# Kernel tuning notes

Measured on AMD Instinct MI355X. Metric: run time of the kernel, lower is better.

The kernel has to match this reference:

```python
import jax, jax.numpy as jnp
import numpy as np

NUM_HEADS = 8
SIGMA = 1.0
LAMBDA_INIT = 0.1
GAMMA_INIT = 0.001


def _pos_encoding(H, W, d_model):
    # 2D sinusoidal encoding: first half encodes x (width), second half y (height)
    d = d_model // 2
    div = jnp.exp(jnp.arange(0, d, 2, dtype=jnp.float32) * (-np.log(10000.0) / d))
    xs = jnp.arange(W, dtype=jnp.float32)[:, None] * div  # (W, d//2)
    ys = jnp.arange(H, dtype=jnp.float32)[:, None] * div  # (H, d//2)
    pe_x = jnp.stack([jnp.sin(xs), jnp.cos(xs)], axis=-1).reshape(W, d)
    pe_y = jnp.stack([jnp.sin(ys), jnp.cos(ys)], axis=-1).reshape(H, d)
    pe = jnp.concatenate([
        jnp.broadcast_to(pe_x[None, :, :], (H, W, d)),
        jnp.broadcast_to(pe_y[:, None, :], (H, W, d)),
    ], axis=-1)
    return pe  # (H, W, d_model)


def _distance_map(H, W, sigma):
    # exp(-euclidean_dist / sigma) between all flattened pixel positions
    yy, xx = jnp.meshgrid(jnp.arange(H, dtype=jnp.float32), jnp.arange(W, dtype=jnp.float32), indexing='ij')
    coords = jnp.stack([yy.reshape(-1), xx.reshape(-1)], axis=-1)  # (HW, 2)
    d2 = jnp.sum((coords[:, None, :] - coords[None, :, :]) ** 2, axis=-1)
    return jnp.exp(-jnp.sqrt(d2) / sigma)  # (HW, HW)


def _conv1x1(x, w, b):
    # 1x1 conv == channel matmul; x: (B,C,H,W), w: (O,C), b: (O,)
    return jnp.einsum('bchw,oc->bohw', x, w) + b[None, :, None, None]


def setup_inputs() -> dict:
    key = jax.random.key(0)
    ks = jax.random.split(key, 9)
    B, C, H, W = 2, 256, 48, 48
    d_model = 256
    inp = {
        'x': jax.random.normal(ks[0], (B, C, H, W), dtype=jnp.float32),
        'Wq': jax.random.normal(ks[1], (d_model, C), dtype=jnp.float32) * 0.01,
        'bq': jnp.zeros((d_model,), dtype=jnp.float32),
        'Wk': jax.random.normal(ks[2], (d_model, C), dtype=jnp.float32) * 0.01,
        'bk': jnp.zeros((d_model,), dtype=jnp.float32),
        'Wv': jax.random.normal(ks[3], (d_model, C), dtype=jnp.float32) * 0.01,
        'bv': jnp.zeros((d_model,), dtype=jnp.float32),
        'Wo': jax.random.normal(ks[4], (C, d_model), dtype=jnp.float32) * 0.01,
        'bo': jnp.zeros((C,), dtype=jnp.float32),
        'lambda_dist': jnp.float32(LAMBDA_INIT),
        'gamma': jnp.float32(GAMMA_INIT),
    }
    return inp


def reference(x, Wq, bq, Wk, bk, Wv, bv, Wo, bo, lambda_dist, gamma):
    B, C, H, W = x.shape
    d_model = Wq.shape[0]
    d_k = d_model // NUM_HEADS
    pe = _pos_encoding(H, W, d_model).transpose(2, 0, 1)[None]  # (1, d_model, H, W)
    dm = _distance_map(H, W, SIGMA)                              # (HW, HW)

    q = _conv1x1(x, Wq, bq) + pe
    k = _conv1x1(x, Wk, bk) + pe
    v = _conv1x1(x, Wv, bv)

    def heads(t):
        return t.reshape(B, NUM_HEADS, d_k, H * W).transpose(0, 1, 3, 2)  # (B,h,HW,d_k)

    Q, K, V = heads(q), heads(k), heads(v)
    scores = jnp.einsum('bhnd,bhmd->bhnm', Q, K) / jnp.sqrt(jnp.float32(d_k))
    scores = scores + (lambda_dist * dm)[None, None]  # 'exp' distance prior bias
    attn = jax.nn.softmax(scores, axis=-1)
    out = jnp.einsum('bhnm,bhmd->bhnd', attn, V)
    out = out.transpose(0, 1, 3, 2).reshape(B, d_model, H, W)
    fused = gamma * out  # simple weighted fusion, single (self) branch
    return x + _conv1x1(fused, Wo, bo)
```

## Files before the change

kernel.cpp:

```cpp
#include <hip/hip_runtime.h>

#define HW 2304
#define SW 48
#define DMODEL 256
#define NHEADS 8
#define DK 32
#define BATCH 2

typedef unsigned short u16;
typedef __attribute__((ext_vector_type(8))) short short8;
typedef __attribute__((ext_vector_type(4))) float f32x4;

__device__ __forceinline__ float bf2f(u16 v) {
  union { unsigned int u; float f; } c; c.u = ((unsigned int)v) << 16; return c.f;
}
__device__ __forceinline__ float lo2f(unsigned int u) {
  union { unsigned int u; float f; } c; c.u = u << 16; return c.f;
}
__device__ __forceinline__ float hi2f(unsigned int u) {
  union { unsigned int u; float f; } c; c.u = u & 0xffff0000u; return c.f;
}
__device__ __forceinline__ u16 f2bf(float f) {
  union { unsigned int u; float f; } c; c.f = f;
  unsigned int u = c.u;
  unsigned int r = (u + 0x7FFFu + ((u >> 16) & 1u)) >> 16;
  return (u16)r;
}
__device__ __forceinline__ unsigned int pkbf(float a, float b) {
  union { float f; unsigned int u; } ca, cb;
  ca.f = a; cb.f = b;
  return __builtin_amdgcn_perm(ca.u, cb.u, 0x03020706u);
}
__device__ __forceinline__ int div48(int n) { return (n * 87382) >> 22; }
__device__ __forceinline__ int swz(int row, int k) {
  return ((row >> 4) << 12) + ((k >> 3) << 7) + ((row & 15) << 3) + (k & 7);
}

__global__ __launch_bounds__(256) void prep_kernel(
    const float* __restrict__ x,
    const float* __restrict__ Wq, const float* __restrict__ Wk,
    const float* __restrict__ Wv, const float* __restrict__ Wo,
    const float* __restrict__ lam_p,
    u16* __restrict__ xt, u16* __restrict__ Wb, u16* __restrict__ et) {
  int bid = blockIdx.x;
  int t = threadIdx.x;
  if (bid < 288) {
    int b = bid / 144, r = bid % 144;
    int c0 = (r / 36) * 64, n0 = (r % 36) * 64;
    __shared__ u16 sh[64][72];
#pragma unroll
    for (int p = 0; p < 4; ++p) {
      int row = (t >> 4) + p * 16;
      int col4 = (t & 15) * 4;
      float4 v = *(const float4*)(x + (size_t)(b * DMODEL + c0 + row) * HW +
                                  n0 + col4);
      sh[col4 + 0][row] = f2bf(v.x);
      sh[col4 + 1][row] = f2bf(v.y);
      sh[col4 + 2][row] = f2bf(v.z);
      sh[col4 + 3][row] = f2bf(v.w);
    }
    __syncthreads();
    u16* xtb = xt + (size_t)b * HW * DMODEL;
#pragma unroll
    for (int q = 0; q < 2; ++q) {
      int nrow = t >> 2;
      int c8 = (t & 3) * 8 + q * 32;
      *(uint4*)(xtb + swz(n0 + nrow, c0 + c8)) = *(const uint4*)&sh[nrow][c8];
    }
  } else if (bid < 544) {
    int idx = (bid - 288) * 1024 + t * 4;
    int which = idx >> 16, off = idx & 65535;
    int m = off >> 8, k = off & 255;
    const float* src = (which == 0) ? Wq : (which == 1) ? Wk
                       : (which == 2) ? Wv : Wo;
    float4 v = *(const float4*)(src + off);
    ushort4 ov;
    ov.x = f2bf(v.x); ov.y = f2bf(v.y); ov.z = f2bf(v.z); ov.w = f2bf(v.w);
    *(ushort4*)(Wb + which * 65536 + swz(m, k)) = ov;
  } else {
    int id = (bid - 544) * 256 + t;
    int flat = id * 8;
    int tile = flat >> 8;
    int within = flat & 255;
    int tm = tile / 144, tq = tile - tm * 144;
    int m = tm * 16 + (within >> 4);
    int q = tq * 16 + (within & 15);
    int ym = div48(m), xm = m - ym * SW;
    int yq = div48(q), xq = q - yq * SW;
    float lam = lam_p[0];
    float dy = (float)(yq - ym);
    float dy2 = dy * dy;
    u16 o[8];
#pragma unroll
    for (int j = 0; j < 8; ++j) {
      float dx = (float)(xq + j - xm);
      o[j] = f2bf(lam * __expf(-sqrtf(dy2 + dx * dx)));
    }
    *(uint4*)(et + flat) = *(const uint4*)o;
  }
}

__global__ __launch_bounds__(256) void qkv_kernel(
    const u16* __restrict__ Wb, const u16* __restrict__ xt,
    const float* __restrict__ bq, const float* __restrict__ bk,
    const float* __restrict__ bv,
    u16* __restrict__ qt, u16* __restrict__ ktb, u16* __restrict__ vb) {
  int t = threadIdx.x;
  int w = t >> 6, lane = t & 63, lo = lane & 15, quad = lane >> 4;
  int n0 = blockIdx.x * 64;
  int mb = blockIdx.y, b = blockIdx.z;
  int which = mb >> 2;
  int mrel0 = (mb & 3) * 64;
  const u16* A = Wb + which * 65536 + ((mrel0 + w * 16) >> 4) * 4096 + lo * 8;
  const float* bias = (which == 0) ? bq : (which == 1) ? bk : bv;
  const u16* Bx = xt + (size_t)b * HW * DMODEL + lo * 8;

  f32x4 acc[4] = {{0.f, 0.f, 0.f, 0.f}, {0.f, 0.f, 0.f, 0.f},
                  {0.f, 0.f, 0.f, 0.f}, {0.f, 0.f, 0.f, 0.f}};
#pragma unroll
  for (int k0 = 0; k0 < DMODEL; k0 += 32) {
    int kblk = ((k0 >> 3) + quad) << 7;
    short8 af = *(const short8*)(A + kblk);
#pragma unroll
    for (int nt = 0; nt < 4; ++nt) {
      short8 bf_ = *(const short8*)(Bx + ((n0 + nt * 16) >> 4) * 4096 + kblk);
      acc[nt] = __builtin_amdgcn_mfma_f32_16x16x32_bf16(af, bf_, acc[nt], 0, 0, 0);
    }
  }

  int mbase = mrel0 + w * 16 + quad * 4;
  if (which == 2) {
#pragma unroll
    for (int reg = 0; reg < 4; ++reg) {
      int mrel = mbase + reg;
      float bi = bias[mrel];
      u16* dst = vb + (size_t)(b * DMODEL + mrel) * HW + n0 + lo;
#pragma unroll
      for (int nt = 0; nt < 4; ++nt) dst[nt * 16] = f2bf(acc[nt][reg] + bi);
    }
  } else {
    float sc = (which == 0) ? 0.17677669529663687f : 1.0f;
    int h = mbase >> 5, d0 = mbase & 31;
    u16* base = ((which == 0) ? qt : ktb) + (size_t)(b * NHEADS + h) * HW * DK;
    float bi[4], dv[4];
    bool usecos[4], usey[4];
#pragma unroll
    for (int reg = 0; reg < 4; ++reg) {
      int mrel = mbase + reg;
      bi[reg] = bias[mrel];
      int oo = mrel & 127;
      dv[reg] = expf(-0.07195578415606394f * (float)(oo & ~1));
      usecos[reg] = (oo & 1);
      usey[reg] = (mrel >= 128);
    }
#pragma unroll
    for (int nt = 0; nt < 4; ++nt) {
      int n = n0 + nt * 16 + lo;
      int yy = div48(n), xx = n - yy * SW;
      ushort4 ov;
      float vals[4];
#pragma unroll
      for (int reg = 0; reg < 4; ++reg) {
        float tv = (usey[reg] ? (float)yy : (float)xx) * dv[reg];
        float pe = usecos[reg] ? cosf(tv) : sinf(tv);
        vals[reg] = (acc[nt][reg] + bi[reg] + pe) * sc;
      }
      ov.x = f2bf(vals[0]); ov.y = f2bf(vals[1]);
      ov.z = f2bf(vals[2]); ov.w = f2bf(vals[3]);
      *(ushort4*)(base + (size_t)n * DK + d0) = ov;
    }
  }
}

__global__ __launch_bounds__(256) void attn_kernel(
    const u16* __restrict__ qt, const u16* __restrict__ ktb,
    const u16* __restrict__ vb, const u16* __restrict__ et,
    u16* __restrict__ po_o, float* __restrict__ po_l) {
  int t = threadIdx.x;
  int w = t >> 6;
  int lane = t & 63;
  int lo = lane & 15, quad = lane >> 4;
  int n0 = blockIdx.x * 64;
  int h = blockIdx.y >> 2, kh = blockIdx.y & 3;
  int b = blockIdx.z;

  __shared__ u16 Ks[2][64 * 40];
  __shared__ u16 Vs[2][32 * 72];

  const u16* qtg = qt + (size_t)(b * NHEADS + h) * HW * DK;
  const u16* ktg = ktb + (size_t)(b * NHEADS + h) * HW * DK;
  const u16* vbg = vb + (size_t)(b * DMODEL + h * DK) * HW;

  short8 qf = *(const short8*)(qtg + (size_t)(n0 + w * 16 + lo) * DK + quad * 8);

  int srow = t >> 2;
  int sks = srow >> 5, srr = srow & 31;
  int sv = (srr < 16) ? (8 * (srr >> 2) + (srr & 3))
                      : (8 * ((srr - 16) >> 2) + 4 + ((srr - 16) & 3));
  int skey = sks * 32 + sv;
  int sc8 = (t & 3) * 8;
  int vdd = t >> 3, vmo = (t & 7) * 8;

  int tq = (n0 >> 4) + w;
  const u16* etw = et + (size_t)tq * 144 * 256 + lo * 16 + (quad & 1) * 8;
  int qh = quad >> 1;

  f32x4 o0 = {0.f, 0.f, 0.f, 0.f}, o1 = {0.f, 0.f, 0.f, 0.f};
  float lsum = 0.f;

  const int kt0 = kh * 9;
  {
    int m0 = kt0 * 64;
    *(uint4*)&Ks[0][srow * 40 + sc8] =
        *(const uint4*)(ktg + (size_t)(m0 + skey) * DK + sc8);
    *(uint4*)&Vs[0][vdd * 72 + vmo] =
        *(const uint4*)(vbg + (size_t)vdd * HW + m0 + vmo);
  }
  __syncthreads();

  for (int i = 0; i < 9; ++i) {
    int cur = i & 1;
    if (i + 1 < 9) {
      int m1 = (kt0 + i + 1) * 64;
      *(uint4*)&Ks[cur ^ 1][srow * 40 + sc8] =
          *(const uint4*)(ktg + (size_t)(m1 + skey) * DK + sc8);
      *(uint4*)&Vs[cur ^ 1][vdd * 72 + vmo] =
          *(const uint4*)(vbg + (size_t)vdd * HW + m1 + vmo);
    }

    int m0 = (kt0 + i) * 64;
    uint4 eb0 = *(const uint4*)(etw + (size_t)((m0 >> 4) + 0 + qh) * 256);
    uint4 eb1 = *(const uint4*)(etw + (size_t)((m0 >> 4) + 2 + qh) * 256);

#pragma unroll
    for (int ks = 0; ks < 2; ++ks) {
      uint4 ebv = ks ? eb1 : eb0;
      short8 kfA = *(const short8*)&Ks[cur][(ks * 32 + lo) * 40 + quad * 8];
      short8 kfB = *(const short8*)&Ks[cur][(ks * 32 + 16 + lo) * 40 + quad * 8];
      f32x4 z = {0.f, 0.f, 0.f, 0.f};
      f32x4 sA = __builtin_amdgcn_mfma_f32_16x16x32_bf16(kfA, qf, z, 0, 0, 0);
      f32x4 sB = __builtin_amdgcn_mfma_f32_16x16x32_bf16(kfB, qf, z, 0, 0, 0);
      float p0 = __expf(sA[0] + lo2f(ebv.x));
      float p1 = __expf(sA[1] + hi2f(ebv.x));
      float p2 = __expf(sA[2] + lo2f(ebv.y));
      float p3 = __expf(sA[3] + hi2f(ebv.y));
      float p4 = __expf(sB[0] + lo2f(ebv.z));
      float p5 = __expf(sB[1] + hi2f(ebv.z));
      float p6 = __expf(sB[2] + lo2f(ebv.w));
      float p7 = __expf(sB[3] + hi2f(ebv.w));
      lsum += ((p0 + p1) + (p2 + p3)) + ((p4 + p5) + (p6 + p7));
      unsigned int pk32[4] = {pkbf(p0, p1), pkbf(p2, p3),
                              pkbf(p4, p5), pkbf(p6, p7)};
      short8 pfrag = *(const short8*)pk32;
      short8 v0 = *(const short8*)&Vs[cur][lo * 72 + ks * 32 + quad * 8];
      o0 = __builtin_amdgcn_mfma_f32_16x16x32_bf16(v0, pfrag, o0, 0, 0, 0);
      short8 v1 = *(const short8*)&Vs[cur][(16 + lo) * 72 + ks * 32 + quad * 8];
      o1 = __builtin_amdgcn_mfma_f32_16x16x32_bf16(v1, pfrag, o1, 0, 0, 0);
    }
    __syncthreads();
  }

  lsum += __shfl_xor(lsum, 16);
  lsum += __shfl_xor(lsum, 32);

  int slot = (b * NHEADS + h) * 36 + blockIdx.x;
  u16* pw = po_o + (size_t)(kh * 576 + slot) * 2048 + w * 512;
  uint2 s0, s1;
  s0.x = pkbf(o0[0], o0[1]); s0.y = pkbf(o0[2], o0[3]);
  s1.x = pkbf(o1[0], o1[1]); s1.y = pkbf(o1[2], o1[3]);
  *(uint2*)(pw + lane * 4) = s0;
  *(uint2*)(pw + 256 + lane * 4) = s1;
  if (quad == 0)
    po_l[(size_t)(kh * 576 + slot) * 64 + w * 16 + lo] = lsum;
}

__global__ __launch_bounds__(256) void reduce_kernel(
    const u16* __restrict__ po_o, const float* __restrict__ po_l,
    u16* __restrict__ aot) {
  int t = threadIdx.x;
  int w = t >> 6, lane = t & 63, lo = lane & 15, quad = lane >> 4;
  int qt_ = blockIdx.x, h = blockIdx.y, b = blockIdx.z;
  int slot = (b * NHEADS + h) * 36 + qt_;

  float s0[4] = {0.f, 0.f, 0.f, 0.f}, s1[4] = {0.f, 0.f, 0.f, 0.f};
  float lt = 0.f;
#pragma unroll
  for (int kh = 0; kh < 4; ++kh) {
    const u16* p = po_o + (size_t)(kh * 576 + slot) * 2048 + w * 512;
    ushort4 a0 = *(const ushort4*)(p + lane * 4);
    ushort4 a1 = *(const ushort4*)(p + 256 + lane * 4);
    s0[0] += bf2f(a0.x); s0[1] += bf2f(a0.y);
    s0[2] += bf2f(a0.z); s0[3] += bf2f(a0.w);
    s1[0] += bf2f(a1.x); s1[1] += bf2f(a1.y);
    s1[2] += bf2f(a1.z); s1[3] += bf2f(a1.w);
    lt += po_l[(size_t)(kh * 576 + slot) * 64 + w * 16 + lo];
  }
  float inv = 1.0f / lt;

  int n = qt_ * 64 + w * 16 + lo;
  u16* aog = aot + (size_t)b * HW * DMODEL;
  ushort4 w0, w1;
  w0.x = f2bf(s0[0] * inv); w0.y = f2bf(s0[1] * inv);
  w0.z = f2bf(s0[2] * inv); w0.w = f2bf(s0[3] * inv);
  w1.x = f2bf(s1[0] * inv); w1.y = f2bf(s1[1] * inv);
  w1.z = f2bf(s1[2] * inv); w1.w = f2bf(s1[3] * inv);
  *(ushort4*)&aog[swz(n, h * DK + quad * 4)] = w0;
  *(ushort4*)&aog[swz(n, h * DK + 16 + quad * 4)] = w1;
}

__global__ __launch_bounds__(256) void out_kernel(
    const float* __restrict__ x, const u16* __restrict__ Wob,
    const float* __restrict__ bo, const float* __restrict__ gp,
    const u16* __restrict__ aot, float* __restrict__ out) {
  int t = threadIdx.x;
  int w = t >> 6, lane = t & 63, lo = lane & 15, quad = lane >> 4;
  int n0 = blockIdx.x * 64;
  int c0 = blockIdx.y * 64;
  int b = blockIdx.z;
  float gamma = gp[0];
  const u16* A = Wob + ((c0 + w * 16) >> 4) * 4096 + lo * 8;
  const u16* Ba = aot + (size_t)b * HW * DMODEL + lo * 8;

  f32x4 acc[4] = {{0.f, 0.f, 0.f, 0.f}, {0.f, 0.f, 0.f, 0.f},
                  {0.f, 0.f, 0.f, 0.f}, {0.f, 0.f, 0.f, 0.f}};
#pragma unroll
  for (int k0 = 0; k0 < DMODEL; k0 += 32) {
    int kblk = ((k0 >> 3) + quad) << 7;
    short8 af = *(const short8*)(A + kblk);
#pragma unroll
    for (int nt = 0; nt < 4; ++nt) {
      short8 bf_ = *(const short8*)(Ba + ((n0 + nt * 16) >> 4) * 4096 + kblk);
      acc[nt] = __builtin_amdgcn_mfma_f32_16x16x32_bf16(af, bf_, acc[nt], 0, 0, 0);
    }
  }

#pragma unroll
  for (int reg = 0; reg < 4; ++reg) {
    int c = c0 + w * 16 + quad * 4 + reg;
    float bi = bo[c];
    const float* xs = x + (size_t)(b * DMODEL + c) * HW + n0 + lo;
    float* os = out + (size_t)(b * DMODEL + c) * HW + n0 + lo;
#pragma unroll
    for (int nt = 0; nt < 4; ++nt)
      os[nt * 16] = xs[nt * 16] + gamma * acc[nt][reg] + bi;
  }
}

extern "C" void kernel_launch(void* const* d_in, const int* in_sizes, int n_in,
                              void* d_out, int out_size, void* d_ws,
                              size_t ws_size, hipStream_t stream) {
  const float* x   = (const float*)d_in[0];
  const float* Wq  = (const float*)d_in[1];
  const float* bq  = (const float*)d_in[2];
  const float* Wk  = (const float*)d_in[3];
  const float* bk  = (const float*)d_in[4];
  const float* Wv  = (const float*)d_in[5];
  const float* bv  = (const float*)d_in[6];
  const float* Wo  = (const float*)d_in[7];
  const float* bo  = (const float*)d_in[8];
  const float* lam = (const float*)d_in[9];
  const float* gam = (const float*)d_in[10];

  char* wsb = (char*)d_ws;
  u16* Wb  = (u16*)(wsb + 36864);
  u16* xt  = (u16*)(wsb + 561152);
  u16* aot = xt;
  u16* qt  = (u16*)(wsb + 2920448);
  u16* ktb = (u16*)(wsb + 5279744);
  u16* vb  = (u16*)(wsb + 7639040);
  u16* et  = (u16*)(wsb + 9998336);
  u16* po_o = (u16*)(wsb + 20615168);
  float* po_l = (float*)(wsb + 30052352);
  float* out = (float*)d_out;

  prep_kernel<<<dim3(3136), 256, 0, stream>>>(x, Wq, Wk, Wv, Wo, lam,
                                              xt, Wb, et);
  qkv_kernel<<<dim3(36, 12, BATCH), 256, 0, stream>>>(Wb, xt, bq, bk, bv,
                                                      qt, ktb, vb);
  attn_kernel<<<dim3(36, 32, BATCH), 256, 0, stream>>>(qt, ktb, vb, et,
                                                       po_o, po_l);
  reduce_kernel<<<dim3(36, 8, BATCH), 256, 0, stream>>>(po_o, po_l, aot);
  out_kernel<<<dim3(36, 4, BATCH), 256, 0, stream>>>(x, Wb + 3 * 65536, bo, gam,
                                                     aot, out);
}
```

Baseline: 129.6 us.

## Compress distance bias table, use exp2 with bias-initialized MFMA, fuse reduce into output GEMM

Replaces the full HW×HW distance-bias table with a compact table indexed by relative (dy, dx) tile offsets, so prep_kernel launches far fewer blocks and the attention kernel reads a small cached table. The attention loop folds log2e into Q and lambda, seeds the score MFMA accumulator with the bias, uses exp2, and computes the row sum with a ones-matrix MFMA instead of scalar adds and shuffles. The separate reduce kernel is removed; out_kernel now merges the four key-split partials per head into shared memory before its projection GEMM, which saves a launch and a round trip through the aot buffer. Fast sin, cos and exp intrinsics are used in the QKV epilogue, which slightly lowers accuracy.

```diff
diff --git a/kernel.cpp b/kernel.cpp
--- a/kernel.cpp
+++ b/kernel.cpp
@@ -31,10 +31,20 @@
   ca.f = a; cb.f = b;
   return __builtin_amdgcn_perm(ca.u, cb.u, 0x03020706u);
 }
+__device__ __forceinline__ float ex2(float x) {
+#if __has_builtin(__builtin_amdgcn_exp2f)
+  return __builtin_amdgcn_exp2f(x);
+#else
+  return __expf(x * 0.6931471805599453f);
+#endif
+}
 __device__ __forceinline__ int div48(int n) { return (n * 87382) >> 22; }
+__device__ __forceinline__ int div3(int n) { return (n * 171) >> 9; }
 __device__ __forceinline__ int swz(int row, int k) {
   return ((row >> 4) << 12) + ((k >> 3) << 7) + ((row & 15) << 3) + (k & 7);
 }
+
+#define LOG2E 1.4426950408889634f
 
 __global__ __launch_bounds__(256) void prep_kernel(
     const float* __restrict__ x,
@@ -79,24 +89,26 @@
     *(ushort4*)(Wb + which * 65536 + swz(m, k)) = ov;
   } else {
     int id = (bid - 544) * 256 + t;
-    int flat = id * 8;
-    int tile = flat >> 8;
-    int within = flat & 255;
-    int tm = tile / 144, tq = tile - tm * 144;
-    int m = tm * 16 + (within >> 4);
-    int q = tq * 16 + (within & 15);
-    int ym = div48(m), xm = m - ym * SW;
-    int yq = div48(q), xq = q - yq * SW;
-    float lam = lam_p[0];
-    float dy = (float)(yq - ym);
-    float dy2 = dy * dy;
-    u16 o[8];
-#pragma unroll
-    for (int j = 0; j < 8; ++j) {
-      float dx = (float)(xq + j - xm);
-      o[j] = f2bf(lam * __expf(-sqrtf(dy2 + dx * dx)));
-    }
-    *(uint4*)(et + flat) = *(const uint4*)o;
+    if (id < 15200) {
+      int flat = id * 8;
+      int tile = flat >> 8;
+      int within = flat & 255;
+      int a = within >> 4;
+      int b0 = within & 15;
+      int dyi = (tile * 205) >> 10;
+      int dp = tile - dyi * 5;
+      float dy = (float)(dyi - 47);
+      float dy2 = dy * dy;
+      int dxb = (dp - 2) * 16 + a - b0;
+      float lam = lam_p[0] * LOG2E;
+      u16 o[8];
+#pragma unroll
+      for (int j = 0; j < 8; ++j) {
+        float dx = (float)(dxb - j);
+        o[j] = f2bf(lam * __expf(-sqrtf(dy2 + dx * dx)));
+      }
+      *(uint4*)(et + flat) = *(const uint4*)o;
+    }
   }
 }
 
@@ -139,7 +151,7 @@
       for (int nt = 0; nt < 4; ++nt) dst[nt * 16] = f2bf(acc[nt][reg] + bi);
     }
   } else {
-    float sc = (which == 0) ? 0.17677669529663687f : 1.0f;
+    float sc = (which == 0) ? (0.17677669529663687f * LOG2E) : 1.0f;
     int h = mbase >> 5, d0 = mbase & 31;
     u16* base = ((which == 0) ? qt : ktb) + (size_t)(b * NHEADS + h) * HW * DK;
     float bi[4], dv[4];
@@ -149,7 +161,7 @@
       int mrel = mbase + reg;
       bi[reg] = bias[mrel];
       int oo = mrel & 127;
-      dv[reg] = expf(-0.07195578415606394f * (float)(oo & ~1));
+      dv[reg] = __expf(-0.07195578415606394f * (float)(oo & ~1));
       usecos[reg] = (oo & 1);
       usey[reg] = (mrel >= 128);
     }
@@ -162,7 +174,7 @@
 #pragma unroll
       for (int reg = 0; reg < 4; ++reg) {
         float tv = (usey[reg] ? (float)yy : (float)xx) * dv[reg];
-        float pe = usecos[reg] ? cosf(tv) : sinf(tv);
+        float pe = usecos[reg] ? __cosf(tv) : __sinf(tv);
         vals[reg] = (acc[nt][reg] + bi[reg] + pe) * sc;
       }
       ov.x = f2bf(vals[0]); ov.y = f2bf(vals[1]);
@@ -202,11 +214,17 @@
   int vdd = t >> 3, vmo = (t & 7) * 8;
 
   int tq = (n0 >> 4) + w;
-  const u16* etw = et + (size_t)tq * 144 * 256 + lo * 16 + (quad & 1) * 8;
   int qh = quad >> 1;
+  int yqt = div3(tq);
+  int qcode = tq + 2 * yqt + 237;
+  const u16* etb = et + lo * 16 + (quad & 1) * 8;
+
+  union { unsigned int u[4]; short8 s; } onesu;
+  onesu.u[0] = onesu.u[1] = onesu.u[2] = onesu.u[3] = 0x3F803F80u;
+  const short8 onesf = onesu.s;
 
   f32x4 o0 = {0.f, 0.f, 0.f, 0.f}, o1 = {0.f, 0.f, 0.f, 0.f};
-  float lsum = 0.f;
+  f32x4 lacc = {0.f, 0.f, 0.f, 0.f};
 
   const int kt0 = kh * 9;
   {
@@ -228,30 +246,27 @@
           *(const uint4*)(vbg + (size_t)vdd * HW + m1 + vmo);
     }
 
-    int m0 = (kt0 + i) * 64;
-    uint4 eb0 = *(const uint4*)(etw + (size_t)((m0 >> 4) + 0 + qh) * 256);
-    uint4 eb1 = *(const uint4*)(etw + (size_t)((m0 >> 4) + 2 + qh) * 256);
+    int tm0 = (kt0 + i) * 4 + qh;
+    int tm1 = tm0 + 2;
+    int ym0 = div3(tm0), ym1 = div3(tm1);
+    uint4 eb0 = *(const uint4*)(etb + (size_t)(qcode - tm0 - 2 * ym0) * 256);
+    uint4 eb1 = *(const uint4*)(etb + (size_t)(qcode - tm1 - 2 * ym1) * 256);
 
 #pragma unroll
     for (int ks = 0; ks < 2; ++ks) {
       uint4 ebv = ks ? eb1 : eb0;
       short8 kfA = *(const short8*)&Ks[cur][(ks * 32 + lo) * 40 + quad * 8];
       short8 kfB = *(const short8*)&Ks[cur][(ks * 32 + 16 + lo) * 40 + quad * 8];
-      f32x4 z = {0.f, 0.f, 0.f, 0.f};
-      f32x4 sA = __builtin_amdgcn_mfma_f32_16x16x32_bf16(kfA, qf, z, 0, 0, 0);
-      f32x4 sB = __builtin_amdgcn_mfma_f32_16x16x32_bf16(kfB, qf, z, 0, 0, 0);
-      float p0 = __expf(sA[0] + lo2f(ebv.x));
-      float p1 = __expf(sA[1] + hi2f(ebv.x));
-      float p2 = __expf(sA[2] + lo2f(ebv.y));
-      float p3 = __expf(sA[3] + hi2f(ebv.y));
-      float p4 = __expf(sB[0] + lo2f(ebv.z));
-      float p5 = __expf(sB[1] + hi2f(ebv.z));
-      float p6 = __expf(sB[2] + lo2f(ebv.w));
-      float p7 = __expf(sB[3] + hi2f(ebv.w));
-      lsum += ((p0 + p1) + (p2 + p3)) + ((p4 + p5) + (p6 + p7));
+      f32x4 zA = {lo2f(ebv.x), hi2f(ebv.x), lo2f(ebv.y), hi2f(ebv.y)};
+      f32x4 zB = {lo2f(ebv.z), hi2f(ebv.z), lo2f(ebv.w), hi2f(ebv.w)};
+      f32x4 sA = __builtin_amdgcn_mfma_f32_16x16x32_bf16(kfA, qf, zA, 0, 0, 0);
+      f32x4 sB = __builtin_amdgcn_mfma_f32_16x16x32_bf16(kfB, qf, zB, 0, 0, 0);
+      float p0 = ex2(sA[0]), p1 = ex2(sA[1]), p2 = ex2(sA[2]), p3 = ex2(sA[3]);
+      float p4 = ex2(sB[0]), p5 = ex2(sB[1]), p6 = ex2(sB[2]), p7 = ex2(sB[3]);
       unsigned int pk32[4] = {pkbf(p0, p1), pkbf(p2, p3),
                               pkbf(p4, p5), pkbf(p6, p7)};
       short8 pfrag = *(const short8*)pk32;
+      lacc = __builtin_amdgcn_mfma_f32_16x16x32_bf16(onesf, pfrag, lacc, 0, 0, 0);
       short8 v0 = *(const short8*)&Vs[cur][lo * 72 + ks * 32 + quad * 8];
       o0 = __builtin_amdgcn_mfma_f32_16x16x32_bf16(v0, pfrag, o0, 0, 0, 0);
       short8 v1 = *(const short8*)&Vs[cur][(16 + lo) * 72 + ks * 32 + quad * 8];
@@ -259,9 +274,6 @@
     }
     __syncthreads();
   }
-
-  lsum += __shfl_xor(lsum, 16);
-  lsum += __shfl_xor(lsum, 32);
 
   int slot = (b * NHEADS + h) * 36 + blockIdx.x;
   u16* pw = po_o + (size_t)(kh * 576 + slot) * 2048 + w * 512;
@@ -271,56 +283,52 @@
   *(uint2*)(pw + lane * 4) = s0;
   *(uint2*)(pw + 256 + lane * 4) = s1;
   if (quad == 0)
-    po_l[(size_t)(kh * 576 + slot) * 64 + w * 16 + lo] = lsum;
-}
-
-__global__ __launch_bounds__(256) void reduce_kernel(
-    const u16* __restrict__ po_o, const float* __restrict__ po_l,
-    u16* __restrict__ aot) {
-  int t = threadIdx.x;
-  int w = t >> 6, lane = t & 63, lo = lane & 15, quad = lane >> 4;
-  int qt_ = blockIdx.x, h = blockIdx.y, b = blockIdx.z;
-  int slot = (b * NHEADS + h) * 36 + qt_;
-
-  float s0[4] = {0.f, 0.f, 0.f, 0.f}, s1[4] = {0.f, 0.f, 0.f, 0.f};
-  float lt = 0.f;
-#pragma unroll
-  for (int kh = 0; kh < 4; ++kh) {
-    const u16* p = po_o + (size_t)(kh * 576 + slot) * 2048 + w * 512;
-    ushort4 a0 = *(const ushort4*)(p + lane * 4);
-    ushort4 a1 = *(const ushort4*)(p + 256 + lane * 4);
-    s0[0] += bf2f(a0.x); s0[1] += bf2f(a0.y);
-    s0[2] += bf2f(a0.z); s0[3] += bf2f(a0.w);
-    s1[0] += bf2f(a1.x); s1[1] += bf2f(a1.y);
-    s1[2] += bf2f(a1.z); s1[3] += bf2f(a1.w);
-    lt += po_l[(size_t)(kh * 576 + slot) * 64 + w * 16 + lo];
-  }
-  float inv = 1.0f / lt;
-
-  int n = qt_ * 64 + w * 16 + lo;
-  u16* aog = aot + (size_t)b * HW * DMODEL;
-  ushort4 w0, w1;
-  w0.x = f2bf(s0[0] * inv); w0.y = f2bf(s0[1] * inv);
-  w0.z = f2bf(s0[2] * inv); w0.w = f2bf(s0[3] * inv);
-  w1.x = f2bf(s1[0] * inv); w1.y = f2bf(s1[1] * inv);
-  w1.z = f2bf(s1[2] * inv); w1.w = f2bf(s1[3] * inv);
-  *(ushort4*)&aog[swz(n, h * DK + quad * 4)] = w0;
-  *(ushort4*)&aog[swz(n, h * DK + 16 + quad * 4)] = w1;
+    po_l[(size_t)(kh * 576 + slot) * 64 + w * 16 + lo] = lacc[0];
 }
 
 __global__ __launch_bounds__(256) void out_kernel(
     const float* __restrict__ x, const u16* __restrict__ Wob,
     const float* __restrict__ bo, const float* __restrict__ gp,
-    const u16* __restrict__ aot, float* __restrict__ out) {
+    const u16* __restrict__ po_o, const float* __restrict__ po_l,
+    float* __restrict__ out) {
   int t = threadIdx.x;
   int w = t >> 6, lane = t & 63, lo = lane & 15, quad = lane >> 4;
-  int n0 = blockIdx.x * 64;
+  int qt_ = blockIdx.x;
   int c0 = blockIdx.y * 64;
   int b = blockIdx.z;
   float gamma = gp[0];
+
+  __shared__ u16 Bt[16384];
+
+#pragma unroll 1
+  for (int h = 0; h < NHEADS; ++h) {
+    int slot = (b * NHEADS + h) * 36 + qt_;
+    float s0[4] = {0.f, 0.f, 0.f, 0.f}, s1[4] = {0.f, 0.f, 0.f, 0.f};
+    float lt = 0.f;
+#pragma unroll
+    for (int kh = 0; kh < 4; ++kh) {
+      const u16* p = po_o + (size_t)(kh * 576 + slot) * 2048 + w * 512;
+      ushort4 a0 = *(const ushort4*)(p + lane * 4);
+      ushort4 a1 = *(const ushort4*)(p + 256 + lane * 4);
+      s0[0] += bf2f(a0.x); s0[1] += bf2f(a0.y);
+      s0[2] += bf2f(a0.z); s0[3] += bf2f(a0.w);
+      s1[0] += bf2f(a1.x); s1[1] += bf2f(a1.y);
+      s1[2] += bf2f(a1.z); s1[3] += bf2f(a1.w);
+      lt += po_l[(size_t)(kh * 576 + slot) * 64 + w * 16 + lo];
+    }
+    float inv = 1.0f / lt;
+    int base = w * 4096 + (h * 4 + (quad >> 1)) * 128 + lo * 8 + (quad & 1) * 4;
+    ushort4 w0, w1;
+    w0.x = f2bf(s0[0] * inv); w0.y = f2bf(s0[1] * inv);
+    w0.z = f2bf(s0[2] * inv); w0.w = f2bf(s0[3] * inv);
+    w1.x = f2bf(s1[0] * inv); w1.y = f2bf(s1[1] * inv);
+    w1.z = f2bf(s1[2] * inv); w1.w = f2bf(s1[3] * inv);
+    *(ushort4*)&Bt[base] = w0;
+    *(ushort4*)&Bt[base + 256] = w1;
+  }
+  __syncthreads();
+
   const u16* A = Wob + ((c0 + w * 16) >> 4) * 4096 + lo * 8;
-  const u16* Ba = aot + (size_t)b * HW * DMODEL + lo * 8;
-
   f32x4 acc[4] = {{0.f, 0.f, 0.f, 0.f}, {0.f, 0.f, 0.f, 0.f},
                   {0.f, 0.f, 0.f, 0.f}, {0.f, 0.f, 0.f, 0.f}};
 #pragma unroll
@@ -329,11 +337,12 @@
     short8 af = *(const short8*)(A + kblk);
 #pragma unroll
     for (int nt = 0; nt < 4; ++nt) {
-      short8 bf_ = *(const short8*)(Ba + ((n0 + nt * 16) >> 4) * 4096 + kblk);
+      short8 bf_ = *(const short8*)&Bt[nt * 4096 + kblk + lo * 8];
       acc[nt] = __builtin_amdgcn_mfma_f32_16x16x32_bf16(af, bf_, acc[nt], 0, 0, 0);
     }
   }
 
+  int n0 = qt_ * 64;
 #pragma unroll
   for (int reg = 0; reg < 4; ++reg) {
     int c = c0 + w * 16 + quad * 4 + reg;
@@ -364,7 +373,6 @@
   char* wsb = (char*)d_ws;
   u16* Wb  = (u16*)(wsb + 36864);
   u16* xt  = (u16*)(wsb + 561152);
-  u16* aot = xt;
   u16* qt  = (u16*)(wsb + 2920448);
   u16* ktb = (u16*)(wsb + 5279744);
   u16* vb  = (u16*)(wsb + 7639040);
@@ -373,13 +381,12 @@
   float* po_l = (float*)(wsb + 30052352);
   float* out = (float*)d_out;
 
-  prep_kernel<<<dim3(3136), 256, 0, stream>>>(x, Wq, Wk, Wv, Wo, lam,
-                                              xt, Wb, et);
+  prep_kernel<<<dim3(604), 256, 0, stream>>>(x, Wq, Wk, Wv, Wo, lam,
+                                             xt, Wb, et);
   qkv_kernel<<<dim3(36, 12, BATCH), 256, 0, stream>>>(Wb, xt, bq, bk, bv,
                                                       qt, ktb, vb);
   attn_kernel<<<dim3(36, 32, BATCH), 256, 0, stream>>>(qt, ktb, vb, et,
                                                        po_o, po_l);
-  reduce_kernel<<<dim3(36, 8, BATCH), 256, 0, stream>>>(po_o, po_l, aot);
   out_kernel<<<dim3(36, 4, BATCH), 256, 0, stream>>>(x, Wb + 3 * 65536, bo, gam,
-                                                     aot, out);
-}
+                                                     po_o, po_l, out);
+}
```

Result: faster. 124.7 us (median of 3 runs) (-3.8%).
